# Optimization experiments

Measured on AMD Instinct MI355X. Metric: run time of the kernel, lower is better.

The kernel has to match this reference:

```python
import jax, jax.numpy as jnp
import numpy as np

B = 64        # number of queries (eg_idx groups)
EPQ = 2048    # edges per query (contiguous blocks, sorted by eg_idx)
E = B * EPQ   # 131072 total edges
D = 128       # n_dims_in; G3 dim = 4*D = 512
N = 50000     # number of visited nodes
K = 256       # max_edges (top-k per query)


def setup_inputs() -> dict:
    key = jax.random.key(0)
    ks = jax.random.split(key, 9)
    scale = np.sqrt(2.0 / (4 * D)).astype(np.float32)
    return {
        "visited_node_score": jax.random.uniform(ks[0], (N,), jnp.float32),
        "visited_node_representation": jax.random.normal(ks[1], (N, D), jnp.float32),
        "rel_emb": jax.random.normal(ks[2], (E, D), jnp.float32),
        "query_src_ts_emb": jax.random.normal(ks[3], (B, D), jnp.float32),
        "query_rel_emb": jax.random.normal(ks[4], (B, D), jnp.float32),
        "Wq": jax.random.normal(ks[5], (4 * D, 4 * D), jnp.float32) * scale,
        "Wk": jax.random.normal(ks[6], (4 * D, 4 * D), jnp.float32) * scale,
        # sorted eg_idx with exactly EPQ edges per query -> regular per-group topk
        "eg_idx": (jnp.arange(E) // EPQ).astype(jnp.int32),
        "node_idx_i": jax.random.randint(ks[7], (E,), 0, N, jnp.int32),
        "node_idx_j": jax.random.randint(ks[8], (E,), 0, N, jnp.int32),
        "k": K,
    }


def segment_softmax(logits, seg, num_segments):
    # numerically-stable softmax over edges sharing the same source node
    m = jax.ops.segment_max(logits, seg, num_segments=num_segments)
    m = jax.lax.stop_gradient(m)
    ex = jnp.exp(logits - m[seg])
    s = jax.ops.segment_sum(ex, seg, num_segments=num_segments)
    return ex / s[seg]


def reference(visited_node_score, visited_node_representation, rel_emb,
              query_src_ts_emb, query_rel_emb, Wq, Wk,
              eg_idx, node_idx_i, node_idx_j, k):
    # gather node / query embeddings per edge (torch index_select)
    hvi = visited_node_representation[node_idx_i]          # [E, D]
    hvj = visited_node_representation[node_idx_j]          # [E, D]
    qs = query_src_ts_emb[eg_idx]                          # [E, D]
    qr = query_rel_emb[eg_idx]                             # [E, D]
    # G3 bilinear: sum(query_proj(cat(left)) * key_proj(cat(right)), -1)
    left = jnp.concatenate([hvi, rel_emb, qs, qr], axis=-1)   # [E, 4D]
    right = jnp.concatenate([hvj, rel_emb, qs, qr], axis=-1)  # [E, 4D]
    logits = jnp.sum((left @ Wq.T) * (right @ Wk.T), axis=-1) # [E]
    # softmax over edges grouped by source node idx (edges[:, -2])
    attn = segment_softmax(logits, node_idx_i, N)              # [E]
    src_score = visited_node_score[node_idx_i]                 # [E]
    target_score = attn * src_score                            # [E]
    # per-query top-k pruning (each query owns a contiguous EPQ block, EPQ > k)
    top_vals, top_idx = jax.lax.top_k(target_score.reshape(B, EPQ), k)
    flat_idx = (top_idx + jnp.arange(B, dtype=top_idx.dtype)[:, None] * EPQ).reshape(-1)
    pruned_attn = attn[flat_idx]                # transition_logits_pruned_softmax
    pruned_src = src_score[flat_idx]            # pruned_src_score
    pruned_tgt = node_idx_j[flat_idx]           # pruned_edges[:, 7]
    # 'sum' node score aggregation: sparse mm == segment_sum of attn * src_score
    updated_node_score = jax.ops.segment_sum(pruned_attn * pruned_src,
                                             pruned_tgt, num_segments=N)
    return updated_node_score
```

## Files before the change

kernel.cpp:

```cpp
#include <hip/hip_runtime.h>
#include <cstddef>

#define EPQ_SHIFT 11
#define KSEL 256

typedef __attribute__((ext_vector_type(8))) short short8v;
typedef __attribute__((ext_vector_type(4))) float float4v;

__device__ __forceinline__ unsigned enc_f(float f) {
  unsigned u = __float_as_uint(f);
  return (u & 0x80000000u) ? ~u : (u | 0x80000000u);
}
__device__ __forceinline__ float dec_f(unsigned k) {
  unsigned u = (k & 0x80000000u) ? (k ^ 0x80000000u) : ~k;
  return __uint_as_float(u);
}
__device__ __forceinline__ unsigned short f2bf(float x) {
  unsigned u = __float_as_uint(x);
  return (unsigned short)((u + 0x7FFFu + ((u >> 16) & 1u)) >> 16);
}

__global__ __launch_bounds__(256) void k1_gemmM(
    const float* __restrict__ Wq, const float* __restrict__ Wk,
    float* __restrict__ M, float* __restrict__ Mt,
    unsigned short* __restrict__ Mh, unsigned short* __restrict__ Ml,
    unsigned short* __restrict__ Mth, unsigned short* __restrict__ Mtl,
    float* __restrict__ outz, float* __restrict__ segsum,
    unsigned* __restrict__ segkey, int N) {
  int tid = threadIdx.x;
  {
    int bid = blockIdx.y * gridDim.x + blockIdx.x;
    for (int idx = bid * 256 + tid; idx < N; idx += 16384) {
      outz[idx] = 0.f;
      segsum[idx] = 0.f;
      segkey[idx] = 0u;
    }
  }
  __shared__ float as[16][64];
  __shared__ float bs[16][64];
  int tx = tid & 15, ty = tid >> 4;
  int c1b = blockIdx.y * 64, c2b = blockIdx.x * 64;
  float acc[4][4] = {};
  for (int k0 = 0; k0 < 512; k0 += 16) {
#pragma unroll
    for (int l = 0; l < 4; ++l) {
      int lin = tid + l * 256;
      int kk = lin >> 6, c = lin & 63;
      as[kk][c] = Wq[(k0 + kk) * 512 + c1b + c];
      bs[kk][c] = Wk[(k0 + kk) * 512 + c2b + c];
    }
    __syncthreads();
#pragma unroll
    for (int kk = 0; kk < 16; ++kk) {
      float a[4], b[4];
#pragma unroll
      for (int m = 0; m < 4; ++m) a[m] = as[kk][ty * 4 + m];
#pragma unroll
      for (int n = 0; n < 4; ++n) b[n] = bs[kk][tx * 4 + n];
#pragma unroll
      for (int m = 0; m < 4; ++m)
#pragma unroll
        for (int n = 0; n < 4; ++n) acc[m][n] += a[m] * b[n];
    }
    __syncthreads();
  }
#pragma unroll
  for (int m = 0; m < 4; ++m)
#pragma unroll
    for (int n = 0; n < 4; ++n) {
      int c1 = c1b + ty * 4 + m, c2 = c2b + tx * 4 + n;
      float v = acc[m][n];
      M[c1 * 512 + c2] = v;
      Mt[c2 * 512 + c1] = v;
      unsigned short h = f2bf(v);
      unsigned short lo = f2bf(v - __uint_as_float((unsigned)h << 16));
      Mh[c1 * 512 + c2] = h;
      Ml[c1 * 512 + c2] = lo;
      Mth[c2 * 512 + c1] = h;
      Mtl[c2 * 512 + c1] = lo;
    }
}


#define STAGE_AB(ASRC, BH, BL, BOFF)                                         \
  {                                                                          \
    const int an = tid >> 2, aq = tid & 3;                                   \
    const float* s = (ASRC);           \
    float4 v0 = *(const float4*)&s[0];                                       \
    float4 v1 = *(const float4*)&s[4];                                       \
    float vv[8] = {v0.x, v0.y, v0.z, v0.w, v1.x, v1.y, v1.z, v1.w};          \
    unsigned hw[4], lw[4];                                                   \
    _Pragma("unroll") for (int j = 0; j < 4; ++j) {                          \
      unsigned short h0 = f2bf(vv[2 * j]);                                   \
      unsigned short h1 = f2bf(vv[2 * j + 1]);                               \
      unsigned short l0 =                                                    \
          f2bf(vv[2 * j] - __uint_as_float((unsigned)h0 << 16));             \
      unsigned short l1 =                                                    \
          f2bf(vv[2 * j + 1] - __uint_as_float((unsigned)h1 << 16));         \
      hw[j] = (unsigned)h0 | ((unsigned)h1 << 16);                           \
      lw[j] = (unsigned)l0 | ((unsigned)l1 << 16);                           \
    }                                                                        \
    int ag = aq ^ ((an >> 1) & 3);                                           \
    *(uint4*)&Ah[an][ag * 8] = make_uint4(hw[0], hw[1], hw[2], hw[3]);       \
    *(uint4*)&Al[an][ag * 8] = make_uint4(lw[0], lw[1], lw[2], lw[3]);       \
    const int bd = tid >> 1, bhalf = tid & 1;                                \
    size_t boff_ = (BOFF);                                                   \
    uint4 q0 = *(const uint4*)&(BH)[boff_];                                  \
    uint4 q1 = *(const uint4*)&(BH)[boff_ + 8];                              \
    uint4 p0 = *(const uint4*)&(BL)[boff_];                                  \
    uint4 p1 = *(const uint4*)&(BL)[boff_ + 8];                              \
    int sw = (bd >> 1) & 3;                                                  \
    int g0 = (bhalf * 2) ^ sw, g1 = (bhalf * 2 + 1) ^ sw;                    \
    *(uint4*)&Bh[bd][g0 * 8] = q0;                                           \
    *(uint4*)&Bh[bd][g1 * 8] = q1;                                           \
    *(uint4*)&Bl[bd][g0 * 8] = p0;                                           \
    *(uint4*)&Bl[bd][g1 * 8] = p1;                                           \
  }

#define MFMA_CHUNK64()                                                       \
  {                                                                          \
    int ln = lane & 15, kq = lane >> 4;                                      \
    short8v ah[2], al[2];                                                    \
    _Pragma("unroll") for (int r = 0; r < 2; ++r) {                          \
      int row = wr2 * 32 + r * 16 + ln;                                      \
      int gg = kq ^ ((row >> 1) & 3);                                        \
      ah[r] = *(const short8v*)&Ah[row][gg * 8];                             \
      al[r] = *(const short8v*)&Al[row][gg * 8];                             \
    }                                                                        \
    _Pragma("unroll") for (int c = 0; c < 4; ++c) {                          \
      int col = wc2 * 64 + c * 16 + ln;                                      \
      int gg = kq ^ ((col >> 1) & 3);                                        \
      short8v bh = *(const short8v*)&Bh[col][gg * 8];                        \
      short8v bl = *(const short8v*)&Bl[col][gg * 8];                        \
      _Pragma("unroll") for (int r = 0; r < 2; ++r) {                        \
        acc[r][c] = __builtin_amdgcn_mfma_f32_16x16x32_bf16(                 \
            ah[r], bh, acc[r][c], 0, 0, 0);                                  \
        acc[r][c] = __builtin_amdgcn_mfma_f32_16x16x32_bf16(                 \
            ah[r], bl, acc[r][c], 0, 0, 0);                                  \
        acc[r][c] = __builtin_amdgcn_mfma_f32_16x16x32_bf16(                 \
            al[r], bh, acc[r][c], 0, 0, 0);                                  \
      }                                                                      \
    }                                                                        \
  }

#define EP_WRITE(GRP)                                                        \
  if (wc2 == ((GRP) >> 1)) {                                                 \
    int ln = lane & 15, kq = lane >> 4;                                      \
    _Pragma("unroll") for (int cc = 0; cc < 2; ++cc) {                       \
      int c = ((GRP) & 1) * 2 + cc;                                          \
      _Pragma("unroll") for (int r = 0; r < 2; ++r)                          \
        _Pragma("unroll") for (int reg = 0; reg < 4; ++reg)                  \
          ep[wr2 * 32 + r * 16 + kq * 4 + reg][cc * 16 + ln] =               \
              acc[r][c][reg];                                                \
  }                                                                          \
  }

__global__ __launch_bounds__(256) void k2m_mfma(
    const float* __restrict__ hv, const unsigned short* __restrict__ Mh,
    const unsigned short* __restrict__ Ml, const unsigned short* __restrict__ Mth,
    const unsigned short* __restrict__ Mtl, float* __restrict__ Tj,
    float* __restrict__ I1, int N) {
  __shared__ char pool[24576];
  unsigned short (*Ah)[32] = (unsigned short(*)[32])pool;
  unsigned short (*Al)[32] = (unsigned short(*)[32])(pool + 4096);
  unsigned short (*Bh)[32] = (unsigned short(*)[32])(pool + 8192);
  unsigned short (*Bl)[32] = (unsigned short(*)[32])(pool + 16384);
  float (*ep)[34] = (float(*)[34])(pool + 8192);

  const int tid = threadIdx.x;
  const int lane = tid & 63;
  const int w = tid >> 6;
  const int wr2 = w >> 1, wc2 = w & 1;
  const int p = blockIdx.x;
  const int n0 = blockIdx.y * 64;
  const unsigned short* bhs = (p == 2) ? Mth : Mh;
  const unsigned short* bls = (p == 2) ? Mtl : Ml;
  const int borow = (p == 0) ? 0 : 128;
  float* outp = (p == 0) ? Tj : (p == 1) ? (Tj + 128) : I1;
  const size_t ostride = (p == 2) ? 128 : 256;

  float4v acc[2][4];
#pragma unroll
  for (int r = 0; r < 2; ++r)
#pragma unroll
    for (int c = 0; c < 4; ++c) acc[r][c] = (float4v){0.f, 0.f, 0.f, 0.f};

  for (int ch = 0; ch < 4; ++ch) {
    __syncthreads();
    {
      int gn = n0 + (tid >> 2);
      gn = gn < N ? gn : N - 1;
      STAGE_AB(hv + (size_t)gn * 128 + ch * 32 + (tid & 3) * 8, bhs, bls,
               (size_t)(borow + (tid >> 1)) * 512 + ch * 32 + (tid & 1) * 16);
    }
    __syncthreads();
    MFMA_CHUNK64();
  }

  for (int g = 0; g < 4; ++g) {
    __syncthreads();
    EP_WRITE(g);
    __syncthreads();
    int row = tid >> 2, part = tid & 3;
    int gn = n0 + row;
    if (gn < N) {
      *(float4*)&outp[(size_t)gn * ostride + g * 32 + part * 8] =
          *(const float4*)&ep[row][part * 8];
      *(float4*)&outp[(size_t)gn * ostride + g * 32 + part * 8 + 4] =
          *(const float4*)&ep[row][part * 8 + 4];
    }
  }
}

__global__ __launch_bounds__(256) void k3_query(const float* __restrict__ qsrc,
                                                const float* __restrict__ qrel,
                                                const float* __restrict__ M,
                                                const float* __restrict__ Mt,
                                                float* __restrict__ wv,
                                                float* __restrict__ uv,
                                                float* __restrict__ yv,
                                                float* __restrict__ cb) {
  __shared__ float qcat[256];
  __shared__ float prt[5][256];
  __shared__ float red[128];
  int b = blockIdx.x, tid = threadIdx.x;
  int d = tid & 127, hc = tid >> 7;
  qcat[tid] = (tid < 128) ? qsrc[b * 128 + tid] : qrel[b * 128 + (tid - 128)];
  __syncthreads();
  float w = 0.f, u = 0.f, y = 0.f, t1 = 0.f, t2 = 0.f;
  for (int c = hc * 128; c < hc * 128 + 128; ++c) {
    float q = qcat[c];
    size_t row = (size_t)(256 + c) * 512;
    w += Mt[row + d] * q;
    u += M[row + d] * q;
    y += (Mt[row + 128 + d] + M[row + 128 + d]) * q;
    t1 += M[row + 256 + d] * q;
    t2 += M[row + 384 + d] * q;
  }
  prt[0][tid] = w; prt[1][tid] = u; prt[2][tid] = y;
  prt[3][tid] = t1; prt[4][tid] = t2;
  __syncthreads();
  if (tid < 128) {
    float wc_ = prt[0][d] + prt[0][128 + d];
    float uc = prt[1][d] + prt[1][128 + d];
    float yc = prt[2][d] + prt[2][128 + d];
    float t1c = prt[3][d] + prt[3][128 + d];
    float t2c = prt[4][d] + prt[4][128 + d];
    wv[b * 128 + d] = wc_;
    uv[b * 128 + d] = uc;
    yv[b * 128 + d] = yc;
    red[d] = qcat[d] * t1c + qcat[128 + d] * t2c;
  }
  __syncthreads();
  for (int s = 64; s > 0; s >>= 1) {
    if (tid < s) red[tid] += red[tid + s];
    __syncthreads();
  }
  if (tid == 0) cb[b] = red[0];
}

__global__ __launch_bounds__(256) void k4m_mfma(
    const float* __restrict__ rel, const unsigned short* __restrict__ Mth,
    const unsigned short* __restrict__ Mtl, const float* __restrict__ yv,
    const float* __restrict__ cbp, float* __restrict__ ec) {
  __shared__ char pool[24576];
  unsigned short (*Ah)[32] = (unsigned short(*)[32])pool;
  unsigned short (*Al)[32] = (unsigned short(*)[32])(pool + 4096);
  unsigned short (*Bh)[32] = (unsigned short(*)[32])(pool + 8192);
  unsigned short (*Bl)[32] = (unsigned short(*)[32])(pool + 16384);
  float (*ep)[34] = (float(*)[34])(pool + 8192);

  const int tid = threadIdx.x;
  const int lane = tid & 63;
  const int w = tid >> 6;
  const int wr2 = w >> 1, wc2 = w & 1;
  const int e0 = blockIdx.x * 64;
  const int b = e0 >> EPQ_SHIFT;

  float4v acc[2][4];
#pragma unroll
  for (int r = 0; r < 2; ++r)
#pragma unroll
    for (int c = 0; c < 4; ++c) acc[r][c] = (float4v){0.f, 0.f, 0.f, 0.f};

  for (int ch = 0; ch < 4; ++ch) {
    __syncthreads();
    STAGE_AB(rel + (size_t)(e0 + (tid >> 2)) * 128 + ch * 32 + (tid & 3) * 8,
             Mth, Mtl,
             (size_t)(128 + (tid >> 1)) * 512 + 128 + ch * 32 + (tid & 1) * 16);
    __syncthreads();
    MFMA_CHUNK64();
  }

  float part = 0.f;
  const int e_loc = tid >> 2, quarter = tid & 3;
  for (int g = 0; g < 4; ++g) {
    __syncthreads();
    EP_WRITE(g);
    __syncthreads();
    const float* rsrc = rel + (size_t)(e0 + e_loc) * 128 + g * 32 + quarter * 8;
    const float* ysrc = yv + b * 128 + g * 32 + quarter * 8;
#pragma unroll
    for (int j = 0; j < 2; ++j) {
      float4 qv = *(const float4*)&ep[e_loc][quarter * 8 + 4 * j];
      float4 rr = *(const float4*)&rsrc[4 * j];
      float4 yy = *(const float4*)&ysrc[4 * j];
      part += (qv.x + yy.x) * rr.x + (qv.y + yy.y) * rr.y +
              (qv.z + yy.z) * rr.z + (qv.w + yy.w) * rr.w;
    }
  }
  part += __shfl_xor(part, 1, 64);
  part += __shfl_xor(part, 2, 64);
  if ((tid & 3) == 0) ec[e0 + e_loc] = part + cbp[b];
}

__global__ __launch_bounds__(256) void k5_logits(const float* __restrict__ rel,
                                                 const float* __restrict__ hv,
                                                 const float* __restrict__ Tj,
                                                 const float* __restrict__ I1,
                                                 const float* __restrict__ wv,
                                                 const float* __restrict__ uv,
                                                 const float* __restrict__ ec,
                                                 const int* __restrict__ node_i,
                                                 const int* __restrict__ node_j,
                                                 float* __restrict__ logits,
                                                 unsigned* __restrict__ segkey) {
  __shared__ float wl[128];
  __shared__ float ul[128];
  int tid = threadIdx.x;
  int e0 = blockIdx.x * 16;
  int b = e0 >> EPQ_SHIFT;
  if (tid < 128) wl[tid] = wv[b * 128 + tid];
  else ul[tid - 128] = uv[b * 128 + (tid - 128)];
  __syncthreads();
  int lane = tid & 15, eg = tid >> 4;
  int e = e0 + eg;
  int i = node_i[e], j = node_j[e];
  int c0 = lane * 8;

  float rr[8], hi[8], hj[8], a0[8], a1[8], ii[8];
  *(float4*)&rr[0] = *(const float4*)&rel[(size_t)e * 128 + c0];
  *(float4*)&rr[4] = *(const float4*)&rel[(size_t)e * 128 + c0 + 4];
  *(float4*)&hi[0] = *(const float4*)&hv[(size_t)i * 128 + c0];
  *(float4*)&hi[4] = *(const float4*)&hv[(size_t)i * 128 + c0 + 4];
  *(float4*)&hj[0] = *(const float4*)&hv[(size_t)j * 128 + c0];
  *(float4*)&hj[4] = *(const float4*)&hv[(size_t)j * 128 + c0 + 4];
  *(float4*)&a0[0] = *(const float4*)&Tj[(size_t)j * 256 + c0];
  *(float4*)&a0[4] = *(const float4*)&Tj[(size_t)j * 256 + c0 + 4];
  *(float4*)&a1[0] = *(const float4*)&Tj[(size_t)j * 256 + 128 + c0];
  *(float4*)&a1[4] = *(const float4*)&Tj[(size_t)j * 256 + 128 + c0 + 4];
  *(float4*)&ii[0] = *(const float4*)&I1[(size_t)i * 128 + c0];
  *(float4*)&ii[4] = *(const float4*)&I1[(size_t)i * 128 + c0 + 4];

  float p = 0.f;
#pragma unroll
  for (int k = 0; k < 8; ++k) {
    p += hi[k] * a0[k];
    p += rr[k] * (a1[k] + ii[k]);
    p += hi[k] * wl[c0 + k];
    p += hj[k] * ul[c0 + k];
  }
#pragma unroll
  for (int m = 8; m >= 1; m >>= 1) p += __shfl_xor(p, m, 64);
  if (lane == 0) {
    float lg = p + ec[e];
    logits[e] = lg;
    atomicMax(&segkey[i], enc_f(lg));
  }
}

__global__ void k6_exp(float* __restrict__ exb, const int* __restrict__ node_i,
                       const unsigned* __restrict__ segkey,
                       float* __restrict__ segsum, int E) {
  int e = blockIdx.x * 256 + threadIdx.x;
  if (e >= E) return;
  int i = node_i[e];
  float m = dec_f(segkey[i]);
  float ex = expf(exb[e] - m);
  exb[e] = ex;
  atomicAdd(&segsum[i], ex);
}

__global__ __launch_bounds__(256) void k7_topk(const float* __restrict__ exb,
                                               const int* __restrict__ node_i,
                                               const int* __restrict__ node_j,
                                               const float* __restrict__ segsum,
                                               const float* __restrict__ score,
                                               float* __restrict__ out) {
  __shared__ unsigned vals[2048];
  __shared__ unsigned hist[256];
  __shared__ unsigned sc[256];
  __shared__ unsigned tie_scan[256];
  __shared__ unsigned sel_info[2];
  int q = blockIdx.x, t = threadIdx.x;
  size_t base = (size_t)q * 2048;
#pragma unroll
  for (int l = 0; l < 8; ++l) {
    int el = t * 8 + l;
    int i = node_i[base + el];
    float tgt = exb[base + el] / segsum[i] * score[i];
    vals[el] = __float_as_uint(tgt);
  }
  __syncthreads();
  unsigned prefix = 0, need = KSEL;
  for (int pass = 3; pass >= 0; --pass) {
    hist[t] = 0;
    __syncthreads();
    int sh = pass * 8;
#pragma unroll
    for (int l = 0; l < 8; ++l) {
      unsigned v = vals[t * 8 + l];
      bool match = (pass == 3) || ((v >> (sh + 8)) == (prefix >> (sh + 8)));
      if (match) atomicAdd(&hist[(v >> sh) & 255u], 1u);
    }
    __syncthreads();
    sc[t] = hist[t];
    __syncthreads();
    for (int off = 1; off < 256; off <<= 1) {
      unsigned add = (t + off < 256) ? sc[t + off] : 0u;
      __syncthreads();
      sc[t] += add;
      __syncthreads();
    }
    unsigned above = sc[t] - hist[t];
    if (above < need && need <= sc[t]) {
      sel_info[0] = (unsigned)t;
      sel_info[1] = need - above;
    }
    __syncthreads();
    prefix |= sel_info[0] << sh;
    need = sel_info[1];
    __syncthreads();
  }
  unsigned T = prefix, r = need;
  unsigned lc = 0;
#pragma unroll
  for (int l = 0; l < 8; ++l)
    if (vals[t * 8 + l] == T) lc++;
  tie_scan[t] = lc;
  __syncthreads();
  unsigned own = lc;
  for (int off = 1; off < 256; off <<= 1) {
    unsigned add = (t >= off) ? tie_scan[t - off] : 0u;
    __syncthreads();
    tie_scan[t] += add;
    __syncthreads();
  }
  unsigned excl = tie_scan[t] - own;
  unsigned cnt = 0;
#pragma unroll
  for (int l = 0; l < 8; ++l) {
    int el = t * 8 + l;
    unsigned v = vals[el];
    bool take = false;
    if (v > T) take = true;
    else if (v == T) { if (excl + cnt < r) take = true; cnt++; }
    if (take) {
      int j = node_j[base + el];
      atomicAdd(&out[j], __uint_as_float(v));
    }
  }
}

extern "C" void kernel_launch(void* const* d_in, const int* in_sizes, int n_in,
                              void* d_out, int out_size, void* d_ws, size_t ws_size,
                              hipStream_t stream) {
  const float* score = (const float*)d_in[0];
  const float* hv    = (const float*)d_in[1];
  const float* rel   = (const float*)d_in[2];
  const float* qsrc  = (const float*)d_in[3];
  const float* qrel  = (const float*)d_in[4];
  const float* Wq    = (const float*)d_in[5];
  const float* Wk    = (const float*)d_in[6];
  const int* node_i  = (const int*)d_in[8];
  const int* node_j  = (const int*)d_in[9];

  const int N = in_sizes[0];
  const int B = in_sizes[3] / 128;
  const int E = in_sizes[2] / 128;

  float* ws = (float*)d_ws;
  float* M  = ws;
  float* Mt = M + 262144;
  float* Tj = Mt + 262144;
  float* I1 = Tj + (size_t)N * 256;
  float* wv = I1 + (size_t)N * 128;
  float* uv = wv + (size_t)B * 128;
  float* yv = uv + (size_t)B * 128;
  float* cb = yv + (size_t)B * 128;
  float* ec = cb + B;
  float* exb = ec + E;
  unsigned* segkey = (unsigned*)(exb + E);
  float* segsum = (float*)(segkey + N);
  unsigned short* Mh  = (unsigned short*)(segsum + N);
  unsigned short* Ml  = Mh + 262144;
  unsigned short* Mth = Ml + 262144;
  unsigned short* Mtl = Mth + 262144;
  float* out = (float*)d_out;

  k1_gemmM<<<dim3(8, 8), 256, 0, stream>>>(Wq, Wk, M, Mt, Mh, Ml, Mth, Mtl,
                                           out, segsum, segkey, N);
  k2m_mfma<<<dim3(3, (N + 63) / 64), 256, 0, stream>>>(hv, Mh, Ml, Mth, Mtl,
                                                       Tj, I1, N);
  k3_query<<<B, 256, 0, stream>>>(qsrc, qrel, M, Mt, wv, uv, yv, cb);
  k4m_mfma<<<E / 64, 256, 0, stream>>>(rel, Mth, Mtl, yv, cb, ec);
  k5_logits<<<E / 16, 256, 0, stream>>>(rel, hv, Tj, I1, wv, uv, ec,
                                        node_i, node_j, exb, segkey);
  k6_exp<<<(E + 255) / 256, 256, 0, stream>>>(exb, node_i, segkey, segsum, E);
  k7_topk<<<B, 256, 0, stream>>>(exb, node_i, node_j, segsum, score, out);
}
```

Measured before the change: 216.2 us.

## Prefetch next K-chunk into registers in MFMA GEMMs and split logits launch

The two MFMA GEMM kernels now load the next 32-wide K chunk of A (fp32) and B (bf16 hi/lo) from global memory into registers while the current chunk's MFMAs run, which is meant to hide global-load latency behind compute. The logits kernel gains an edge-offset parameter and is launched twice over the two halves of the edges. The prefetch raises register pressure. The split launch adds a launch without an obvious benefit, since both halves sit on the same stream.

```diff
diff --git a/kernel.cpp b/kernel.cpp
--- a/kernel.cpp
+++ b/kernel.cpp
@@ -82,13 +82,26 @@
 }
 
 
-#define STAGE_AB(ASRC, BH, BL, BOFF)                                         \
+#define K_DECL()                                                             \
+  float4 ra0, ra1;                                                           \
+  uint4 rbh0, rbh1, rbl0, rbl1;                                              \
+  const int an = tid >> 2, aq = tid & 3;                                     \
+  const int ag = aq ^ ((an >> 1) & 3);                                       \
+  const int bd = tid >> 1, bhalf = tid & 1;                                  \
+  const int bsw = (bd >> 1) & 3;                                             \
+  const int bg0 = (bhalf * 2) ^ bsw, bg1 = (bhalf * 2 + 1) ^ bsw;
+
+#define K_LOAD(CH)                                                           \
+  ra0 = *(const float4*)&asrc[(CH) * 32];                                    \
+  ra1 = *(const float4*)&asrc[(CH) * 32 + 4];                                \
+  rbh0 = *(const uint4*)&bhsrc[(CH) * 32];                                   \
+  rbh1 = *(const uint4*)&bhsrc[(CH) * 32 + 8];                               \
+  rbl0 = *(const uint4*)&blsrc[(CH) * 32];                                   \
+  rbl1 = *(const uint4*)&blsrc[(CH) * 32 + 8];
+
+#define K_WRITE()                                                            \
   {                                                                          \
-    const int an = tid >> 2, aq = tid & 3;                                   \
-    const float* s = (ASRC);           \
-    float4 v0 = *(const float4*)&s[0];                                       \
-    float4 v1 = *(const float4*)&s[4];                                       \
-    float vv[8] = {v0.x, v0.y, v0.z, v0.w, v1.x, v1.y, v1.z, v1.w};          \
+    float vv[8] = {ra0.x, ra0.y, ra0.z, ra0.w, ra1.x, ra1.y, ra1.z, ra1.w};  \
     unsigned hw[4], lw[4];                                                   \
     _Pragma("unroll") for (int j = 0; j < 4; ++j) {                          \
       unsigned short h0 = f2bf(vv[2 * j]);                                   \
@@ -100,21 +113,12 @@
       hw[j] = (unsigned)h0 | ((unsigned)h1 << 16);                           \
       lw[j] = (unsigned)l0 | ((unsigned)l1 << 16);                           \
     }                                                                        \
-    int ag = aq ^ ((an >> 1) & 3);                                           \
     *(uint4*)&Ah[an][ag * 8] = make_uint4(hw[0], hw[1], hw[2], hw[3]);       \
     *(uint4*)&Al[an][ag * 8] = make_uint4(lw[0], lw[1], lw[2], lw[3]);       \
-    const int bd = tid >> 1, bhalf = tid & 1;                                \
-    size_t boff_ = (BOFF);                                                   \
-    uint4 q0 = *(const uint4*)&(BH)[boff_];                                  \
-    uint4 q1 = *(const uint4*)&(BH)[boff_ + 8];                              \
-    uint4 p0 = *(const uint4*)&(BL)[boff_];                                  \
-    uint4 p1 = *(const uint4*)&(BL)[boff_ + 8];                              \
-    int sw = (bd >> 1) & 3;                                                  \
-    int g0 = (bhalf * 2) ^ sw, g1 = (bhalf * 2 + 1) ^ sw;                    \
-    *(uint4*)&Bh[bd][g0 * 8] = q0;                                           \
-    *(uint4*)&Bh[bd][g1 * 8] = q1;                                           \
-    *(uint4*)&Bl[bd][g0 * 8] = p0;                                           \
-    *(uint4*)&Bl[bd][g1 * 8] = p1;                                           \
+    *(uint4*)&Bh[bd][bg0 * 8] = rbh0;                                        \
+    *(uint4*)&Bh[bd][bg1 * 8] = rbh1;                                        \
+    *(uint4*)&Bl[bd][bg0 * 8] = rbl0;                                        \
+    *(uint4*)&Bl[bd][bg1 * 8] = rbl1;                                        \
   }
 
 #define MFMA_CHUNK64()                                                       \
@@ -143,6 +147,27 @@
     }                                                                        \
   }
 
+#define K_MAIN_LOOP()                                                        \
+  K_LOAD(0);                                                                 \
+  _Pragma("unroll") for (int ch = 0; ch < 4; ++ch) {                         \
+    __syncthreads();                                                         \
+    K_WRITE();                                                               \
+    float4 na0, na1;                                                         \
+    uint4 nbh0, nbh1, nbl0, nbl1;                                            \
+    if (ch < 3) {        \
+      na0 = *(const float4*)&asrc[(ch + 1) * 32];                            \
+      na1 = *(const float4*)&asrc[(ch + 1) * 32 + 4];                        \
+      nbh0 = *(const uint4*)&bhsrc[(ch + 1) * 32];                           \
+      nbh1 = *(const uint4*)&bhsrc[(ch + 1) * 32 + 8];                       \
+      nbl0 = *(const uint4*)&blsrc[(ch + 1) * 32];                           \
+      nbl1 = *(const uint4*)&blsrc[(ch + 1) * 32 + 8];                       \
+    }                                                                        \
+    __syncthreads();                                                         \
+    MFMA_CHUNK64();                                                          \
+    ra0 = na0; ra1 = na1;                                                    \
+    rbh0 = nbh0; rbh1 = nbh1; rbl0 = nbl0; rbl1 = nbl1;                      \
+  }
+
 #define EP_WRITE(GRP)                                                        \
   if (wc2 == ((GRP) >> 1)) {                                                 \
     int ln = lane & 15, kq = lane >> 4;                                      \
@@ -185,28 +210,25 @@
 #pragma unroll
     for (int c = 0; c < 4; ++c) acc[r][c] = (float4v){0.f, 0.f, 0.f, 0.f};
 
-  for (int ch = 0; ch < 4; ++ch) {
-    __syncthreads();
-    {
-      int gn = n0 + (tid >> 2);
-      gn = gn < N ? gn : N - 1;
-      STAGE_AB(hv + (size_t)gn * 128 + ch * 32 + (tid & 3) * 8, bhs, bls,
-               (size_t)(borow + (tid >> 1)) * 512 + ch * 32 + (tid & 1) * 16);
-    }
-    __syncthreads();
-    MFMA_CHUNK64();
-  }
+  K_DECL();
+  int gn = n0 + an;
+  gn = gn < N ? gn : N - 1;
+  const float* asrc = hv + (size_t)gn * 128 + aq * 8;
+  const unsigned short* bhsrc = bhs + (size_t)(borow + bd) * 512 + bhalf * 16;
+  const unsigned short* blsrc = bls + (size_t)(borow + bd) * 512 + bhalf * 16;
+
+  K_MAIN_LOOP();
 
   for (int g = 0; g < 4; ++g) {
     __syncthreads();
     EP_WRITE(g);
     __syncthreads();
     int row = tid >> 2, part = tid & 3;
-    int gn = n0 + row;
-    if (gn < N) {
-      *(float4*)&outp[(size_t)gn * ostride + g * 32 + part * 8] =
+    int on = n0 + row;
+    if (on < N) {
+      *(float4*)&outp[(size_t)on * ostride + g * 32 + part * 8] =
           *(const float4*)&ep[row][part * 8];
-      *(float4*)&outp[(size_t)gn * ostride + g * 32 + part * 8 + 4] =
+      *(float4*)&outp[(size_t)on * ostride + g * 32 + part * 8 + 4] =
           *(const float4*)&ep[row][part * 8 + 4];
     }
   }
@@ -283,14 +305,12 @@
 #pragma unroll
     for (int c = 0; c < 4; ++c) acc[r][c] = (float4v){0.f, 0.f, 0.f, 0.f};
 
-  for (int ch = 0; ch < 4; ++ch) {
-    __syncthreads();
-    STAGE_AB(rel + (size_t)(e0 + (tid >> 2)) * 128 + ch * 32 + (tid & 3) * 8,
-             Mth, Mtl,
-             (size_t)(128 + (tid >> 1)) * 512 + 128 + ch * 32 + (tid & 1) * 16);
-    __syncthreads();
-    MFMA_CHUNK64();
-  }
+  K_DECL();
+  const float* asrc = rel + (size_t)(e0 + an) * 128 + aq * 8;
+  const unsigned short* bhsrc = Mth + (size_t)(128 + bd) * 512 + 128 + bhalf * 16;
+  const unsigned short* blsrc = Mtl + (size_t)(128 + bd) * 512 + 128 + bhalf * 16;
+
+  K_MAIN_LOOP();
 
   float part = 0.f;
   const int e_loc = tid >> 2, quarter = tid & 3;
@@ -324,11 +344,12 @@
                                                  const int* __restrict__ node_i,
                                                  const int* __restrict__ node_j,
                                                  float* __restrict__ logits,
-                                                 unsigned* __restrict__ segkey) {
+                                                 unsigned* __restrict__ segkey,
+                                                 int e_base) {
   __shared__ float wl[128];
   __shared__ float ul[128];
   int tid = threadIdx.x;
-  int e0 = blockIdx.x * 16;
+  int e0 = e_base + blockIdx.x * 16;
   int b = e0 >> EPQ_SHIFT;
   if (tid < 128) wl[tid] = wv[b * 128 + tid];
   else ul[tid - 128] = uv[b * 128 + (tid - 128)];
@@ -504,8 +525,10 @@
                                                        Tj, I1, N);
   k3_query<<<B, 256, 0, stream>>>(qsrc, qrel, M, Mt, wv, uv, yv, cb);
   k4m_mfma<<<E / 64, 256, 0, stream>>>(rel, Mth, Mtl, yv, cb, ec);
-  k5_logits<<<E / 16, 256, 0, stream>>>(rel, hv, Tj, I1, wv, uv, ec,
-                                        node_i, node_j, exb, segkey);
+  k5_logits<<<E / 32, 256, 0, stream>>>(rel, hv, Tj, I1, wv, uv, ec,
+                                        node_i, node_j, exb, segkey, 0);
+  k5_logits<<<E / 32, 256, 0, stream>>>(rel, hv, Tj, I1, wv, uv, ec,
+                                        node_i, node_j, exb, segkey, E / 2);
   k6_exp<<<(E + 255) / 256, 256, 0, stream>>>(exb, node_i, segkey, segsum, E);
   k7_topk<<<B, 256, 0, stream>>>(exb, node_i, node_j, segsum, score, out);
 }
```

Measured after the change: 214.4 us. No clear change (-0.8%).

## Fuse three k2 projections per node tile, prefetch B in registers, warp-shuffle top-k scans

Applied to the files above, without the earlier changes.

The k2 kernel now handles all three projection outputs in one block per 64-node tile. It converts the hv rows to split bf16 once into a larger shared buffer instead of redoing this per projection block, and it register-prefetches the next B chunk while the current one is consumed. k4 gains the same register double-buffering of A and B chunks. The top-k kernel swaps its shared-memory Hillis-Steele scans, which need many barriers, for wavefront shuffle scans plus a small per-wave total. This costs more LDS per block in k2 (48KB) and fewer blocks, which may reduce occupancy and parallelism.

```diff
diff --git a/kernel.cpp b/kernel.cpp
--- a/kernel.cpp
+++ b/kernel.cpp
@@ -81,68 +81,6 @@
     }
 }
 
-
-#define STAGE_AB(ASRC, BH, BL, BOFF)                                         \
-  {                                                                          \
-    const int an = tid >> 2, aq = tid & 3;                                   \
-    const float* s = (ASRC);           \
-    float4 v0 = *(const float4*)&s[0];                                       \
-    float4 v1 = *(const float4*)&s[4];                                       \
-    float vv[8] = {v0.x, v0.y, v0.z, v0.w, v1.x, v1.y, v1.z, v1.w};          \
-    unsigned hw[4], lw[4];                                                   \
-    _Pragma("unroll") for (int j = 0; j < 4; ++j) {                          \
-      unsigned short h0 = f2bf(vv[2 * j]);                                   \
-      unsigned short h1 = f2bf(vv[2 * j + 1]);                               \
-      unsigned short l0 =                                                    \
-          f2bf(vv[2 * j] - __uint_as_float((unsigned)h0 << 16));             \
-      unsigned short l1 =                                                    \
-          f2bf(vv[2 * j + 1] - __uint_as_float((unsigned)h1 << 16));         \
-      hw[j] = (unsigned)h0 | ((unsigned)h1 << 16);                           \
-      lw[j] = (unsigned)l0 | ((unsigned)l1 << 16);                           \
-    }                                                                        \
-    int ag = aq ^ ((an >> 1) & 3);                                           \
-    *(uint4*)&Ah[an][ag * 8] = make_uint4(hw[0], hw[1], hw[2], hw[3]);       \
-    *(uint4*)&Al[an][ag * 8] = make_uint4(lw[0], lw[1], lw[2], lw[3]);       \
-    const int bd = tid >> 1, bhalf = tid & 1;                                \
-    size_t boff_ = (BOFF);                                                   \
-    uint4 q0 = *(const uint4*)&(BH)[boff_];                                  \
-    uint4 q1 = *(const uint4*)&(BH)[boff_ + 8];                              \
-    uint4 p0 = *(const uint4*)&(BL)[boff_];                                  \
-    uint4 p1 = *(const uint4*)&(BL)[boff_ + 8];                              \
-    int sw = (bd >> 1) & 3;                                                  \
-    int g0 = (bhalf * 2) ^ sw, g1 = (bhalf * 2 + 1) ^ sw;                    \
-    *(uint4*)&Bh[bd][g0 * 8] = q0;                                           \
-    *(uint4*)&Bh[bd][g1 * 8] = q1;                                           \
-    *(uint4*)&Bl[bd][g0 * 8] = p0;                                           \
-    *(uint4*)&Bl[bd][g1 * 8] = p1;                                           \
-  }
-
-#define MFMA_CHUNK64()                                                       \
-  {                                                                          \
-    int ln = lane & 15, kq = lane >> 4;                                      \
-    short8v ah[2], al[2];                                                    \
-    _Pragma("unroll") for (int r = 0; r < 2; ++r) {                          \
-      int row = wr2 * 32 + r * 16 + ln;                                      \
-      int gg = kq ^ ((row >> 1) & 3);                                        \
-      ah[r] = *(const short8v*)&Ah[row][gg * 8];                             \
-      al[r] = *(const short8v*)&Al[row][gg * 8];                             \
-    }                                                                        \
-    _Pragma("unroll") for (int c = 0; c < 4; ++c) {                          \
-      int col = wc2 * 64 + c * 16 + ln;                                      \
-      int gg = kq ^ ((col >> 1) & 3);                                        \
-      short8v bh = *(const short8v*)&Bh[col][gg * 8];                        \
-      short8v bl = *(const short8v*)&Bl[col][gg * 8];                        \
-      _Pragma("unroll") for (int r = 0; r < 2; ++r) {                        \
-        acc[r][c] = __builtin_amdgcn_mfma_f32_16x16x32_bf16(                 \
-            ah[r], bh, acc[r][c], 0, 0, 0);                                  \
-        acc[r][c] = __builtin_amdgcn_mfma_f32_16x16x32_bf16(                 \
-            ah[r], bl, acc[r][c], 0, 0, 0);                                  \
-        acc[r][c] = __builtin_amdgcn_mfma_f32_16x16x32_bf16(                 \
-            al[r], bh, acc[r][c], 0, 0, 0);                                  \
-      }                                                                      \
-    }                                                                        \
-  }
-
 #define EP_WRITE(GRP)                                                        \
   if (wc2 == ((GRP) >> 1)) {                                                 \
     int ln = lane & 15, kq = lane >> 4;                                      \
@@ -155,59 +93,140 @@
   }                                                                          \
   }
 
-__global__ __launch_bounds__(256) void k2m_mfma(
+__global__ __launch_bounds__(256) void k2m3_mfma(
     const float* __restrict__ hv, const unsigned short* __restrict__ Mh,
     const unsigned short* __restrict__ Ml, const unsigned short* __restrict__ Mth,
     const unsigned short* __restrict__ Mtl, float* __restrict__ Tj,
     float* __restrict__ I1, int N) {
-  __shared__ char pool[24576];
-  unsigned short (*Ah)[32] = (unsigned short(*)[32])pool;
-  unsigned short (*Al)[32] = (unsigned short(*)[32])(pool + 4096);
-  unsigned short (*Bh)[32] = (unsigned short(*)[32])(pool + 8192);
-  unsigned short (*Bl)[32] = (unsigned short(*)[32])(pool + 16384);
-  float (*ep)[34] = (float(*)[34])(pool + 8192);
+  __shared__ char pool[49152];
+  unsigned short (*Ah4)[64][32] = (unsigned short(*)[64][32])pool;
+  unsigned short (*Al4)[64][32] = (unsigned short(*)[64][32])(pool + 16384);
+  unsigned short (*Bh)[32] = (unsigned short(*)[32])(pool + 32768);
+  unsigned short (*Bl)[32] = (unsigned short(*)[32])(pool + 40960);
+  float (*ep)[34] = (float(*)[34])(pool + 32768);
 
   const int tid = threadIdx.x;
   const int lane = tid & 63;
   const int w = tid >> 6;
   const int wr2 = w >> 1, wc2 = w & 1;
-  const int p = blockIdx.x;
-  const int n0 = blockIdx.y * 64;
-  const unsigned short* bhs = (p == 2) ? Mth : Mh;
-  const unsigned short* bls = (p == 2) ? Mtl : Ml;
-  const int borow = (p == 0) ? 0 : 128;
-  float* outp = (p == 0) ? Tj : (p == 1) ? (Tj + 128) : I1;
-  const size_t ostride = (p == 2) ? 128 : 256;
-
-  float4v acc[2][4];
-#pragma unroll
-  for (int r = 0; r < 2; ++r)
-#pragma unroll
-    for (int c = 0; c < 4; ++c) acc[r][c] = (float4v){0.f, 0.f, 0.f, 0.f};
-
-  for (int ch = 0; ch < 4; ++ch) {
-    __syncthreads();
-    {
-      int gn = n0 + (tid >> 2);
-      gn = gn < N ? gn : N - 1;
-      STAGE_AB(hv + (size_t)gn * 128 + ch * 32 + (tid & 3) * 8, bhs, bls,
-               (size_t)(borow + (tid >> 1)) * 512 + ch * 32 + (tid & 1) * 16);
-    }
-    __syncthreads();
-    MFMA_CHUNK64();
-  }
-
-  for (int g = 0; g < 4; ++g) {
-    __syncthreads();
-    EP_WRITE(g);
-    __syncthreads();
-    int row = tid >> 2, part = tid & 3;
-    int gn = n0 + row;
-    if (gn < N) {
-      *(float4*)&outp[(size_t)gn * ostride + g * 32 + part * 8] =
-          *(const float4*)&ep[row][part * 8];
-      *(float4*)&outp[(size_t)gn * ostride + g * 32 + part * 8 + 4] =
-          *(const float4*)&ep[row][part * 8 + 4];
+  const int n0 = blockIdx.x * 64;
+
+  {
+    const int an = tid >> 2, aq = tid & 3;
+    const int ag = aq ^ ((an >> 1) & 3);
+    int gn = n0 + an;
+    gn = gn < N ? gn : N - 1;
+    const float* asrc = hv + (size_t)gn * 128 + aq * 8;
+#pragma unroll
+    for (int ch = 0; ch < 4; ++ch) {
+      float4 v0 = *(const float4*)&asrc[ch * 32];
+      float4 v1 = *(const float4*)&asrc[ch * 32 + 4];
+      float vv[8] = {v0.x, v0.y, v0.z, v0.w, v1.x, v1.y, v1.z, v1.w};
+      unsigned hw[4], lw[4];
+#pragma unroll
+      for (int j = 0; j < 4; ++j) {
+        unsigned short h0 = f2bf(vv[2 * j]);
+        unsigned short h1 = f2bf(vv[2 * j + 1]);
+        unsigned short l0 = f2bf(vv[2 * j] - __uint_as_float((unsigned)h0 << 16));
+        unsigned short l1 = f2bf(vv[2 * j + 1] - __uint_as_float((unsigned)h1 << 16));
+        hw[j] = (unsigned)h0 | ((unsigned)h1 << 16);
+        lw[j] = (unsigned)l0 | ((unsigned)l1 << 16);
+      }
+      *(uint4*)&Ah4[ch][an][ag * 8] = make_uint4(hw[0], hw[1], hw[2], hw[3]);
+      *(uint4*)&Al4[ch][an][ag * 8] = make_uint4(lw[0], lw[1], lw[2], lw[3]);
+    }
+  }
+
+  const int bd = tid >> 1, bhalf = tid & 1;
+  const int bsw = (bd >> 1) & 3;
+  const int bg0 = (bhalf * 2) ^ bsw, bg1 = (bhalf * 2 + 1) ^ bsw;
+  const size_t bcol = (size_t)bd * 512 + bhalf * 16;
+  const unsigned short* bh0 = Mh + bcol;
+  const unsigned short* bh1 = Mh + (size_t)128 * 512 + bcol;
+  const unsigned short* bh2 = Mth + (size_t)128 * 512 + bcol;
+  const unsigned short* bl0 = Ml + bcol;
+  const unsigned short* bl1 = Ml + (size_t)128 * 512 + bcol;
+  const unsigned short* bl2 = Mtl + (size_t)128 * 512 + bcol;
+
+  uint4 rbh0 = *(const uint4*)&bh0[0];
+  uint4 rbh1 = *(const uint4*)&bh0[8];
+  uint4 rbl0 = *(const uint4*)&bl0[0];
+  uint4 rbl1 = *(const uint4*)&bl0[8];
+
+#pragma unroll
+  for (int p = 0; p < 3; ++p) {
+    float* outp = (p == 0) ? Tj : (p == 1) ? (Tj + 128) : I1;
+    const size_t ostride = (p == 2) ? 128 : 256;
+    float4v acc[2][4];
+#pragma unroll
+    for (int r = 0; r < 2; ++r)
+#pragma unroll
+      for (int c = 0; c < 4; ++c) acc[r][c] = (float4v){0.f, 0.f, 0.f, 0.f};
+
+#pragma unroll
+    for (int ch = 0; ch < 4; ++ch) {
+      __syncthreads();
+      *(uint4*)&Bh[bd][bg0 * 8] = rbh0;
+      *(uint4*)&Bh[bd][bg1 * 8] = rbh1;
+      *(uint4*)&Bl[bd][bg0 * 8] = rbl0;
+      *(uint4*)&Bl[bd][bg1 * 8] = rbl1;
+      uint4 nh0, nh1, nl0, nl1;
+      {
+        const int s = p * 4 + ch + 1;
+        if (s < 12) {
+          const int np = s >> 2, nch = s & 3;
+          const unsigned short* nbh = (np == 0) ? bh0 : (np == 1) ? bh1 : bh2;
+          const unsigned short* nbl = (np == 0) ? bl0 : (np == 1) ? bl1 : bl2;
+          nh0 = *(const uint4*)&nbh[nch * 32];
+          nh1 = *(const uint4*)&nbh[nch * 32 + 8];
+          nl0 = *(const uint4*)&nbl[nch * 32];
+          nl1 = *(const uint4*)&nbl[nch * 32 + 8];
+        }
+      }
+      __syncthreads();
+      {
+        int ln = lane & 15, kq = lane >> 4;
+        short8v ah[2], al[2];
+#pragma unroll
+        for (int r = 0; r < 2; ++r) {
+          int row = wr2 * 32 + r * 16 + ln;
+          int gg = kq ^ ((row >> 1) & 3);
+          ah[r] = *(const short8v*)&Ah4[ch][row][gg * 8];
+          al[r] = *(const short8v*)&Al4[ch][row][gg * 8];
+        }
+#pragma unroll
+        for (int c = 0; c < 4; ++c) {
+          int col = wc2 * 64 + c * 16 + ln;
+          int gg = kq ^ ((col >> 1) & 3);
+          short8v bh = *(const short8v*)&Bh[col][gg * 8];
+          short8v bl = *(const short8v*)&Bl[col][gg * 8];
+#pragma unroll
+          for (int r = 0; r < 2; ++r) {
+            acc[r][c] = __builtin_amdgcn_mfma_f32_16x16x32_bf16(ah[r], bh,
+                                                                acc[r][c], 0, 0, 0);
+            acc[r][c] = __builtin_amdgcn_mfma_f32_16x16x32_bf16(ah[r], bl,
+                                                                acc[r][c], 0, 0, 0);
+            acc[r][c] = __builtin_amdgcn_mfma_f32_16x16x32_bf16(al[r], bh,
+                                                                acc[r][c], 0, 0, 0);
+          }
+        }
+      }
+      rbh0 = nh0; rbh1 = nh1; rbl0 = nl0; rbl1 = nl1;
+    }
+
+#pragma unroll
+    for (int g = 0; g < 4; ++g) {
+      __syncthreads();
+      EP_WRITE(g);
+      __syncthreads();
+      int row = tid >> 2, part = tid & 3;
+      int on = n0 + row;
+      if (on < N) {
+        *(float4*)&outp[(size_t)on * ostride + g * 32 + part * 8] =
+            *(const float4*)&ep[row][part * 8];
+        *(float4*)&outp[(size_t)on * ostride + g * 32 + part * 8 + 4] =
+            *(const float4*)&ep[row][part * 8 + 4];
+      }
     }
   }
 }
@@ -283,17 +302,89 @@
 #pragma unroll
     for (int c = 0; c < 4; ++c) acc[r][c] = (float4v){0.f, 0.f, 0.f, 0.f};
 
+  const int an = tid >> 2, aq = tid & 3;
+  const int ag = aq ^ ((an >> 1) & 3);
+  const int bd = tid >> 1, bhalf = tid & 1;
+  const int bsw = (bd >> 1) & 3;
+  const int bg0 = (bhalf * 2) ^ bsw, bg1 = (bhalf * 2 + 1) ^ bsw;
+  const float* asrc = rel + (size_t)(e0 + an) * 128 + aq * 8;
+  const unsigned short* bhsrc = Mth + (size_t)(128 + bd) * 512 + 128 + bhalf * 16;
+  const unsigned short* blsrc = Mtl + (size_t)(128 + bd) * 512 + 128 + bhalf * 16;
+
+  float4 ra0 = *(const float4*)&asrc[0];
+  float4 ra1 = *(const float4*)&asrc[4];
+  uint4 rbh0 = *(const uint4*)&bhsrc[0];
+  uint4 rbh1 = *(const uint4*)&bhsrc[8];
+  uint4 rbl0 = *(const uint4*)&blsrc[0];
+  uint4 rbl1 = *(const uint4*)&blsrc[8];
+
+#pragma unroll
   for (int ch = 0; ch < 4; ++ch) {
     __syncthreads();
-    STAGE_AB(rel + (size_t)(e0 + (tid >> 2)) * 128 + ch * 32 + (tid & 3) * 8,
-             Mth, Mtl,
-             (size_t)(128 + (tid >> 1)) * 512 + 128 + ch * 32 + (tid & 1) * 16);
-    __syncthreads();
-    MFMA_CHUNK64();
+    {
+      float vv[8] = {ra0.x, ra0.y, ra0.z, ra0.w, ra1.x, ra1.y, ra1.z, ra1.w};
+      unsigned hw[4], lw[4];
+#pragma unroll
+      for (int j = 0; j < 4; ++j) {
+        unsigned short h0 = f2bf(vv[2 * j]);
+        unsigned short h1 = f2bf(vv[2 * j + 1]);
+        unsigned short l0 = f2bf(vv[2 * j] - __uint_as_float((unsigned)h0 << 16));
+        unsigned short l1 = f2bf(vv[2 * j + 1] - __uint_as_float((unsigned)h1 << 16));
+        hw[j] = (unsigned)h0 | ((unsigned)h1 << 16);
+        lw[j] = (unsigned)l0 | ((unsigned)l1 << 16);
+      }
+      *(uint4*)&Ah[an][ag * 8] = make_uint4(hw[0], hw[1], hw[2], hw[3]);
+      *(uint4*)&Al[an][ag * 8] = make_uint4(lw[0], lw[1], lw[2], lw[3]);
+      *(uint4*)&Bh[bd][bg0 * 8] = rbh0;
+      *(uint4*)&Bh[bd][bg1 * 8] = rbh1;
+      *(uint4*)&Bl[bd][bg0 * 8] = rbl0;
+      *(uint4*)&Bl[bd][bg1 * 8] = rbl1;
+    }
+    float4 na0, na1;
+    uint4 nbh0, nbh1, nbl0, nbl1;
+    if (ch < 3) {
+      na0 = *(const float4*)&asrc[(ch + 1) * 32];
+      na1 = *(const float4*)&asrc[(ch + 1) * 32 + 4];
+      nbh0 = *(const uint4*)&bhsrc[(ch + 1) * 32];
+      nbh1 = *(const uint4*)&bhsrc[(ch + 1) * 32 + 8];
+      nbl0 = *(const uint4*)&blsrc[(ch + 1) * 32];
+      nbl1 = *(const uint4*)&blsrc[(ch + 1) * 32 + 8];
+    }
+    __syncthreads();
+    {
+      int ln = lane & 15, kq = lane >> 4;
+      short8v ah[2], al[2];
+#pragma unroll
+      for (int r = 0; r < 2; ++r) {
+        int row = wr2 * 32 + r * 16 + ln;
+        int gg = kq ^ ((row >> 1) & 3);
+        ah[r] = *(const short8v*)&Ah[row][gg * 8];
+        al[r] = *(const short8v*)&Al[row][gg * 8];
+      }
+#pragma unroll
+      for (int c = 0; c < 4; ++c) {
+        int col = wc2 * 64 + c * 16 + ln;
+        int gg = kq ^ ((col >> 1) & 3);
+        short8v bh = *(const short8v*)&Bh[col][gg * 8];
+        short8v bl = *(const short8v*)&Bl[col][gg * 8];
+#pragma unroll
+        for (int r = 0; r < 2; ++r) {
+          acc[r][c] = __builtin_amdgcn_mfma_f32_16x16x32_bf16(ah[r], bh,
+                                                              acc[r][c], 0, 0, 0);
+          acc[r][c] = __builtin_amdgcn_mfma_f32_16x16x32_bf16(ah[r], bl,
+                                                              acc[r][c], 0, 0, 0);
+          acc[r][c] = __builtin_amdgcn_mfma_f32_16x16x32_bf16(al[r], bh,
+                                                              acc[r][c], 0, 0, 0);
+        }
+      }
+    }
+    ra0 = na0; ra1 = na1;
+    rbh0 = nbh0; rbh1 = nbh1; rbl0 = nbl0; rbl1 = nbl1;
   }
 
   float part = 0.f;
   const int e_loc = tid >> 2, quarter = tid & 3;
+#pragma unroll
   for (int g = 0; g < 4; ++g) {
     __syncthreads();
     EP_WRITE(g);
@@ -389,10 +480,10 @@
                                                float* __restrict__ out) {
   __shared__ unsigned vals[2048];
   __shared__ unsigned hist[256];
-  __shared__ unsigned sc[256];
-  __shared__ unsigned tie_scan[256];
+  __shared__ unsigned wtot[4];
   __shared__ unsigned sel_info[2];
   int q = blockIdx.x, t = threadIdx.x;
+  int lane = t & 63, w = t >> 6;
   size_t base = (size_t)q * 2048;
 #pragma unroll
   for (int l = 0; l < 8; ++l) {
@@ -414,16 +505,19 @@
       if (match) atomicAdd(&hist[(v >> sh) & 255u], 1u);
     }
     __syncthreads();
-    sc[t] = hist[t];
-    __syncthreads();
-    for (int off = 1; off < 256; off <<= 1) {
-      unsigned add = (t + off < 256) ? sc[t + off] : 0u;
-      __syncthreads();
-      sc[t] += add;
-      __syncthreads();
-    }
-    unsigned above = sc[t] - hist[t];
-    if (above < need && need <= sc[t]) {
+    unsigned myh = hist[t];
+    unsigned v = myh;
+#pragma unroll
+    for (int off = 1; off < 64; off <<= 1) {
+      unsigned o = __shfl_down(v, off, 64);
+      if (lane + off < 64) v += o;
+    }
+    if (lane == 0) wtot[w] = v;
+    __syncthreads();
+    unsigned sct = v;
+    for (int ww = w + 1; ww < 4; ++ww) sct += wtot[ww];
+    unsigned above = sct - myh;
+    if (above < need && need <= sct) {
       sel_info[0] = (unsigned)t;
       sel_info[1] = need - above;
     }
@@ -437,27 +531,28 @@
 #pragma unroll
   for (int l = 0; l < 8; ++l)
     if (vals[t * 8 + l] == T) lc++;
-  tie_scan[t] = lc;
+  unsigned v = lc;
+#pragma unroll
+  for (int off = 1; off < 64; off <<= 1) {
+    unsigned o = __shfl_up(v, off, 64);
+    if (lane >= off) v += o;
+  }
+  if (lane == 63) wtot[w] = v;
   __syncthreads();
-  unsigned own = lc;
-  for (int off = 1; off < 256; off <<= 1) {
-    unsigned add = (t >= off) ? tie_scan[t - off] : 0u;
-    __syncthreads();
-    tie_scan[t] += add;
-    __syncthreads();
-  }
-  unsigned excl = tie_scan[t] - own;
+  unsigned pre = 0;
+  for (int ww = 0; ww < w; ++ww) pre += wtot[ww];
+  unsigned excl = v + pre - lc;
   unsigned cnt = 0;
 #pragma unroll
   for (int l = 0; l < 8; ++l) {
     int el = t * 8 + l;
-    unsigned v = vals[el];
+    unsigned vv = vals[el];
     bool take = false;
-    if (v > T) take = true;
-    else if (v == T) { if (excl + cnt < r) take = true; cnt++; }
+    if (vv > T) take = true;
+    else if (vv == T) { if (excl + cnt < r) take = true; cnt++; }
     if (take) {
       int j = node_j[base + el];
-      atomicAdd(&out[j], __uint_as_float(v));
+      atomicAdd(&out[j], __uint_as_float(vv));
     }
   }
 }
@@ -500,8 +595,7 @@
 
   k1_gemmM<<<dim3(8, 8), 256, 0, stream>>>(Wq, Wk, M, Mt, Mh, Ml, Mth, Mtl,
                                            out, segsum, segkey, N);
-  k2m_mfma<<<dim3(3, (N + 63) / 64), 256, 0, stream>>>(hv, Mh, Ml, Mth, Mtl,
-                                                       Tj, I1, N);
+  k2m3_mfma<<<(N + 63) / 64, 256, 0, stream>>>(hv, Mh, Ml, Mth, Mtl, Tj, I1, N);
   k3_query<<<B, 256, 0, stream>>>(qsrc, qrel, M, Mt, wv, uv, yv, cb);
   k4m_mfma<<<E / 64, 256, 0, stream>>>(rel, Mth, Mtl, yv, cb, ec);
   k5_logits<<<E / 16, 256, 0, stream>>>(rel, hv, Tj, I1, wv, uv, ec,
```

Result: no change. 214.2 us (-1.0%).
